# Performance work log

Hardware: AMD Instinct MI355X
Metric: run time of the kernel (lower is better)

Reference implementation:

```python
import jax, jax.numpy as jnp
import numpy as np

DIM = 768
HEADS = 12
HEAD_DIM = DIM // HEADS
HIDDEN = int(DIM * 2.0)
EPS = 1e-5


def layer_norm(x, g, b):
    mu = jnp.mean(x, axis=-1, keepdims=True)
    var = jnp.var(x, axis=-1, keepdims=True)
    return (x - mu) * jax.lax.rsqrt(var + EPS) * g + b


def setup_inputs() -> dict:
    key = jax.random.key(0)
    ks = jax.random.split(key, 10)
    B, N = 8, 1024
    s = 0.02
    return {
        "x": jax.random.normal(ks[0], (B, N, DIM), jnp.float32),
        "rpe_bias": jax.random.normal(ks[1], (HEADS, N, N), jnp.float32),
        # weights stored as (in, out); equals torch Linear weight transposed
        "qkv_w": jax.random.normal(ks[2], (DIM, 3 * DIM), jnp.float32) * s,
        "proj_w": jax.random.normal(ks[3], (DIM, DIM), jnp.float32) * s,
        "proj_b": jnp.zeros((DIM,), jnp.float32),
        "ln1_g": jnp.ones((DIM,), jnp.float32),
        "ln1_b": jnp.zeros((DIM,), jnp.float32),
        "ln2_g": jnp.ones((DIM,), jnp.float32),
        "ln2_b": jnp.zeros((DIM,), jnp.float32),
        "fc1_w": jax.random.normal(ks[4], (DIM, HIDDEN), jnp.float32) * s,
        "fc1_b": jnp.zeros((HIDDEN,), jnp.float32),
        "fc2_w": jax.random.normal(ks[5], (HIDDEN, DIM), jnp.float32) * s,
        "fc2_b": jnp.zeros((DIM,), jnp.float32),
    }


def reference(x, rpe_bias, qkv_w, proj_w, proj_b, ln1_g, ln1_b, ln2_g, ln2_b,
              fc1_w, fc1_b, fc2_w, fc2_b):
    B, N, C = x.shape
    scale = HEAD_DIM ** -0.5

    # ---- attention branch (pre-norm) ----
    h = layer_norm(x, ln1_g, ln1_b)
    qkv = h @ qkv_w                                   # [B,N,3C]
    qkv = qkv.reshape(B, N, 3, HEADS, HEAD_DIM)
    q = jnp.transpose(qkv[:, :, 0], (0, 2, 1, 3))     # [B,H,N,D]
    k = jnp.transpose(qkv[:, :, 1], (0, 2, 1, 3))
    v = jnp.transpose(qkv[:, :, 2], (0, 2, 1, 3))
    attn = jnp.einsum('bhnd,bhmd->bhnm', q, k) * scale + rpe_bias[None]
    attn = jax.nn.softmax(attn, axis=-1)
    o = jnp.einsum('bhnm,bhmd->bhnd', attn, v)        # [B,H,N,D]
    o = jnp.transpose(o, (0, 2, 1, 3)).reshape(B, N, C)
    x = x + (o @ proj_w + proj_b)

    # ---- MLP branch (pre-norm) ----
    h = layer_norm(x, ln2_g, ln2_b)
    h = jax.nn.gelu(h @ fc1_w + fc1_b, approximate=False)
    x = x + (h @ fc2_w + fc2_b)
    return x
```

## Files before the change

kernel.cpp:

```cpp
#include <hip/hip_runtime.h>

typedef __bf16 bf16;
typedef __bf16 bf16x8 __attribute__((ext_vector_type(8)));
typedef float f32x4 __attribute__((ext_vector_type(4)));

#define DIM 768
#define HEADS 12
#define HD 64
#define HIDDEN 1536
#define BB 8
#define NN 1024
#define ROWS (BB*NN)

__device__ __forceinline__ void gload_lds16(const void* g, void* l) {
  __builtin_amdgcn_global_load_lds(
      (const __attribute__((address_space(1))) void*)g,
      (__attribute__((address_space(3))) void*)l, 16, 0, 0);
}

__global__ __launch_bounds__(256) void ln_kernel(
    const float* __restrict__ x, const float* __restrict__ gw,
    const float* __restrict__ bw, bf16* __restrict__ out)
{
  const int row = blockIdx.x;
  const int tid = threadIdx.x;
  const float* xr = x + (size_t)row * DIM;
  float v0 = xr[tid], v1 = xr[tid + 256], v2 = xr[tid + 512];
  float s1 = v0 + v1 + v2;
  float s2 = v0*v0 + v1*v1 + v2*v2;
#pragma unroll
  for (int off = 1; off < 64; off <<= 1) {
    s1 += __shfl_xor(s1, off);
    s2 += __shfl_xor(s2, off);
  }
  __shared__ float red[8];
  const int w = tid >> 6, lane = tid & 63;
  if (lane == 0) { red[w] = s1; red[4 + w] = s2; }
  __syncthreads();
  s1 = red[0] + red[1] + red[2] + red[3];
  s2 = red[4] + red[5] + red[6] + red[7];
  const float mu = s1 * (1.f / DIM);
  const float rstd = rsqrtf(s2 * (1.f / DIM) - mu * mu + 1e-5f);
  bf16* orow = out + (size_t)row * DIM;
  orow[tid]       = (bf16)((v0 - mu) * rstd * gw[tid]       + bw[tid]);
  orow[tid + 256] = (bf16)((v1 - mu) * rstd * gw[tid + 256] + bw[tid + 256]);
  orow[tid + 512] = (bf16)((v2 - mu) * rstd * gw[tid + 512] + bw[tid + 512]);
}

__global__ void wtrans_kernel(const float* __restrict__ in, bf16* __restrict__ out,
                              int K, int N)
{
  __shared__ float t[32][33];
  const int tx = threadIdx.x, ty = threadIdx.y;
  const int n0 = blockIdx.x * 32, k0 = blockIdx.y * 32;
#pragma unroll
  for (int i = 0; i < 32; i += 8)
    t[ty + i][tx] = in[(size_t)(k0 + ty + i) * N + n0 + tx];
  __syncthreads();
#pragma unroll
  for (int i = 0; i < 32; i += 8)
    out[(size_t)(n0 + ty + i) * K + k0 + tx] = (bf16)t[tx][ty + i];
}

template<int EPI>
__global__ __launch_bounds__(256, 2) void gemm128(
    const bf16* __restrict__ A, const bf16* __restrict__ Bt,
    int M, int N, int K,
    const float* __restrict__ bias, const float* __restrict__ resid,
    void* __restrict__ o0, void* __restrict__ o1, void* __restrict__ o2)
{
  __shared__ bf16 sA[128 * 64];
  __shared__ bf16 sB[128 * 64];
  const int tid = threadIdx.x;
  const int lane = tid & 63, w = tid >> 6;
  const int wrow = w >> 1, wcol = w & 1;
  const int m0 = blockIdx.y * 128, n0 = blockIdx.x * 128;
  const int l15 = lane & 15, l4 = lane >> 4;

  f32x4 acc[4][4] = {};

  const int crow = lane >> 3;
  const int cbyte = (lane & 7) * 16;
  const int ksteps = K >> 6;
  for (int kt = 0; kt < ksteps; ++kt) {
    const int k0 = kt << 6;
    __syncthreads();
#pragma unroll
    for (int c2 = 0; c2 < 4; ++c2) {
      const int c = (w << 2) + c2;
      const int r = (c << 3) + crow;
      gload_lds16((const char*)(A + (size_t)(m0 + r) * K + k0) + cbyte,
                  (char*)sA + c * 1024);
      gload_lds16((const char*)(Bt + (size_t)(n0 + r) * K + k0) + cbyte,
                  (char*)sB + c * 1024);
    }
    __syncthreads();
#pragma unroll
    for (int kk = 0; kk < 64; kk += 32) {
      bf16x8 af[4], bfv[4];
#pragma unroll
      for (int mf = 0; mf < 4; ++mf)
        af[mf] = *(const bf16x8*)(sA + (wrow * 64 + mf * 16 + l15) * 64 + kk + l4 * 8);
#pragma unroll
      for (int nf = 0; nf < 4; ++nf)
        bfv[nf] = *(const bf16x8*)(sB + (wcol * 64 + nf * 16 + l15) * 64 + kk + l4 * 8);
#pragma unroll
      for (int mf = 0; mf < 4; ++mf)
#pragma unroll
        for (int nf = 0; nf < 4; ++nf)
          acc[mf][nf] = __builtin_amdgcn_mfma_f32_16x16x32_bf16(af[mf], bfv[nf], acc[mf][nf], 0, 0, 0);
    }
  }

#pragma unroll
  for (int mf = 0; mf < 4; ++mf) {
    const int rbase = m0 + wrow * 64 + mf * 16 + l4 * 4;
#pragma unroll
    for (int nf = 0; nf < 4; ++nf) {
      const int colbase = n0 + wcol * 64 + nf * 16;
      const int col = colbase + l15;
      if constexpr (EPI == 0) {
        const int seg = colbase / 768;
        const int hh_ = (colbase - seg * 768) >> 6;
        const int dd = (colbase & 63) + l15;
        const int b_ = rbase >> 10;
        const int ns = rbase & 1023;
        const size_t gh = (size_t)(b_ * HEADS + hh_);
        bf16* Qb = (bf16*)o0; bf16* Kb = (bf16*)o1; bf16* Vtb = (bf16*)o2;
        if (seg == 0) {
#pragma unroll
          for (int rg = 0; rg < 4; ++rg)
            Qb[(gh * NN + ns + rg) * HD + dd] = (bf16)(acc[mf][nf][rg] * 0.125f);
        } else if (seg == 1) {
#pragma unroll
          for (int rg = 0; rg < 4; ++rg)
            Kb[(gh * NN + ns + rg) * HD + dd] = (bf16)acc[mf][nf][rg];
        } else {
          union { ushort4 u4; unsigned short us[4]; } pk;
#pragma unroll
          for (int rg = 0; rg < 4; ++rg)
            pk.us[rg] = __builtin_bit_cast(unsigned short, (bf16)acc[mf][nf][rg]);
          *(ushort4*)(Vtb + (gh * HD + dd) * NN + ns) = pk.u4;
        }
      } else if constexpr (EPI == 1 || EPI == 3) {
        float* outp = (float*)o0;
#pragma unroll
        for (int rg = 0; rg < 4; ++rg) {
          const size_t idx = (size_t)(rbase + rg) * N + col;
          outp[idx] = acc[mf][nf][rg] + bias[col] + resid[idx];
        }
      } else {
        bf16* outp = (bf16*)o0;
#pragma unroll
        for (int rg = 0; rg < 4; ++rg) {
          float v = acc[mf][nf][rg] + bias[col];
          float gl = 0.5f * v * (1.0f + erff(v * 0.70710678118654752f));
          outp[(size_t)(rbase + rg) * N + col] = (bf16)gl;
        }
      }
    }
  }
}

__global__ __launch_bounds__(256, 2) void attn_kernel(
    const bf16* __restrict__ Qb, const bf16* __restrict__ Kb,
    const bf16* __restrict__ Vtb, const float* __restrict__ rpe,
    bf16* __restrict__ o_attn)
{
  __shared__ bf16 sK[64 * 64];
  __shared__ bf16 sV[64 * 64];
  __shared__ bf16 sP[4 * 16 * 64];
  const int tid = threadIdx.x;
  const int lane = tid & 63, w = tid >> 6;
  const int l15 = lane & 15, l4 = lane >> 4;
  const int bid = blockIdx.x;
  const int g = bid >> 4, qt = bid & 15;
  const int b_ = g / HEADS, h_ = g % HEADS;
  const int qbase = qt * 64 + w * 16;

  bf16x8 qf[2];
  {
    const bf16* qp = Qb + ((size_t)g * NN + qbase + l15) * HD + l4 * 8;
    qf[0] = *(const bf16x8*)qp;
    qf[1] = *(const bf16x8*)(qp + 32);
  }

  f32x4 oacc[4] = {};
  float m_r[4] = {-1e30f, -1e30f, -1e30f, -1e30f};
  float l_r[4] = {};
  const float* rpe_h = rpe + (size_t)h_ * NN * NN;

  const int crow = lane >> 3;
  const int scol = ((lane & 7) * 16) ^ ((crow & 7) << 4);

  for (int kv0 = 0; kv0 < NN; kv0 += 64) {
    __syncthreads();
#pragma unroll
    for (int c2 = 0; c2 < 2; ++c2) {
      const int c = w * 2 + c2;
      const int r = c * 8 + crow;
      gload_lds16((const char*)(Kb + ((size_t)g * NN + kv0) * HD) + r * 128 + scol,
                  (char*)sK + c * 1024);
      gload_lds16((const char*)(Vtb + ((size_t)g * HD + r) * NN + kv0) + scol,
                  (char*)sV + c * 1024);
    }
    __syncthreads();

    f32x4 s[4] = {};
#pragma unroll
    for (int kh = 0; kh < 2; ++kh) {
#pragma unroll
      for (int nf = 0; nf < 4; ++nf) {
        const int n_ = nf * 16 + l15;
        const bf16x8 kf = *(const bf16x8*)((const char*)sK + n_ * 128 +
                            (((kh * 32 + l4 * 8) * 2) ^ ((n_ & 7) << 4)));
        s[nf] = __builtin_amdgcn_mfma_f32_16x16x32_bf16(qf[kh], kf, s[nf], 0, 0, 0);
      }
    }
    float rm[4] = {-1e30f, -1e30f, -1e30f, -1e30f};
#pragma unroll
    for (int nf = 0; nf < 4; ++nf) {
      const int kvc = kv0 + nf * 16 + l15;
#pragma unroll
      for (int rg = 0; rg < 4; ++rg) {
        const int qr = qbase + l4 * 4 + rg;
        float v = s[nf][rg] + rpe_h[(size_t)qr * NN + kvc];
        s[nf][rg] = v;
        rm[rg] = fmaxf(rm[rg], v);
      }
    }
#pragma unroll
    for (int off = 1; off <= 8; off <<= 1)
#pragma unroll
      for (int rg = 0; rg < 4; ++rg)
        rm[rg] = fmaxf(rm[rg], __shfl_xor(rm[rg], off));
    float al[4];
#pragma unroll
    for (int rg = 0; rg < 4; ++rg) {
      const float mn = fmaxf(m_r[rg], rm[rg]);
      al[rg] = __expf(m_r[rg] - mn);
      m_r[rg] = mn;
    }
    float rs[4] = {};
#pragma unroll
    for (int nf = 0; nf < 4; ++nf)
#pragma unroll
      for (int rg = 0; rg < 4; ++rg) {
        const float p = __expf(s[nf][rg] - m_r[rg]);
        rs[rg] += p;
        const int r = l4 * 4 + rg;
        const int cb = (nf * 16 + l15) * 2;
        *(bf16*)((char*)sP + w * 2048 + r * 128 + (cb ^ ((r & 7) << 4))) = (bf16)p;
      }
#pragma unroll
    for (int off = 1; off <= 8; off <<= 1)
#pragma unroll
      for (int rg = 0; rg < 4; ++rg)
        rs[rg] += __shfl_xor(rs[rg], off);
#pragma unroll
    for (int rg = 0; rg < 4; ++rg)
      l_r[rg] = l_r[rg] * al[rg] + rs[rg];
#pragma unroll
    for (int df = 0; df < 4; ++df)
#pragma unroll
      for (int rg = 0; rg < 4; ++rg)
        oacc[df][rg] *= al[rg];
    __syncthreads();

#pragma unroll
    for (int kh = 0; kh < 2; ++kh) {
      const bf16x8 pf = *(const bf16x8*)((const char*)sP + w * 2048 + l15 * 128 +
                          (((kh * 32 + l4 * 8) * 2) ^ ((l15 & 7) << 4)));
#pragma unroll
      for (int df = 0; df < 4; ++df) {
        const int d_ = df * 16 + l15;
        const bf16x8 vf = *(const bf16x8*)((const char*)sV + d_ * 128 +
                            (((kh * 32 + l4 * 8) * 2) ^ ((d_ & 7) << 4)));
        oacc[df] = __builtin_amdgcn_mfma_f32_16x16x32_bf16(pf, vf, oacc[df], 0, 0, 0);
      }
    }
  }

#pragma unroll
  for (int rg = 0; rg < 4; ++rg) {
    const float inv = 1.0f / l_r[rg];
    const int qr = qbase + l4 * 4 + rg;
    bf16* orow = o_attn + ((size_t)(b_ * NN) + qr) * DIM + h_ * HD;
#pragma unroll
    for (int df = 0; df < 4; ++df)
      orow[df * 16 + l15] = (bf16)(oacc[df][rg] * inv);
  }
}

extern "C" void kernel_launch(void* const* d_in, const int* in_sizes, int n_in,
                              void* d_out, int out_size, void* d_ws, size_t ws_size,
                              hipStream_t stream)
{
  const float* x      = (const float*)d_in[0];
  const float* rpe    = (const float*)d_in[1];
  const float* qkv_w  = (const float*)d_in[2];
  const float* proj_w = (const float*)d_in[3];
  const float* proj_b = (const float*)d_in[4];
  const float* ln1_g  = (const float*)d_in[5];
  const float* ln1_b  = (const float*)d_in[6];
  const float* ln2_g  = (const float*)d_in[7];
  const float* ln2_b  = (const float*)d_in[8];
  const float* fc1_w  = (const float*)d_in[9];
  const float* fc1_b  = (const float*)d_in[10];
  const float* fc2_w  = (const float*)d_in[11];
  const float* fc2_b  = (const float*)d_in[12];
  float* out = (float*)d_out;

  char* ws = (char*)d_ws;
  size_t off = 0;
  bf16* qkv_wT  = (bf16*)(ws + off); off += (size_t)2304 * 768 * 2;
  bf16* proj_wT = (bf16*)(ws + off); off += (size_t)768 * 768 * 2;
  bf16* fc1_wT  = (bf16*)(ws + off); off += (size_t)1536 * 768 * 2;
  bf16* fc2_wT  = (bf16*)(ws + off); off += (size_t)768 * 1536 * 2;
  bf16* hbuf    = (bf16*)(ws + off); off += (size_t)ROWS * DIM * 2;
  bf16* Qb      = (bf16*)(ws + off); off += (size_t)96 * NN * HD * 2;
  bf16* Kb      = (bf16*)(ws + off); off += (size_t)96 * NN * HD * 2;
  bf16* Vtb     = (bf16*)(ws + off); off += (size_t)96 * HD * NN * 2;
  float* x1     = (float*)(ws + off); off += (size_t)ROWS * DIM * 4;
  bf16* o_attn = hbuf;
  bf16* h2 = Qb;
  bf16* hh = Kb;

  dim3 tb(32, 8);
  wtrans_kernel<<<dim3(2304 / 32, 768 / 32), tb, 0, stream>>>(qkv_w, qkv_wT, 768, 2304);
  wtrans_kernel<<<dim3(768 / 32, 768 / 32),  tb, 0, stream>>>(proj_w, proj_wT, 768, 768);
  wtrans_kernel<<<dim3(1536 / 32, 768 / 32), tb, 0, stream>>>(fc1_w, fc1_wT, 768, 1536);
  wtrans_kernel<<<dim3(768 / 32, 1536 / 32), tb, 0, stream>>>(fc2_w, fc2_wT, 1536, 768);

  ln_kernel<<<ROWS, 256, 0, stream>>>(x, ln1_g, ln1_b, hbuf);
  gemm128<0><<<dim3(2304 / 128, ROWS / 128), 256, 0, stream>>>(
      hbuf, qkv_wT, ROWS, 2304, 768, nullptr, nullptr, (void*)Qb, (void*)Kb, (void*)Vtb);
  attn_kernel<<<96 * 16, 256, 0, stream>>>(Qb, Kb, Vtb, rpe, o_attn);
  gemm128<1><<<dim3(768 / 128, ROWS / 128), 256, 0, stream>>>(
      o_attn, proj_wT, ROWS, 768, 768, proj_b, x, (void*)x1, nullptr, nullptr);
  ln_kernel<<<ROWS, 256, 0, stream>>>(x1, ln2_g, ln2_b, h2);
  gemm128<2><<<dim3(1536 / 128, ROWS / 128), 256, 0, stream>>>(
      h2, fc1_wT, ROWS, 1536, 768, fc1_b, nullptr, (void*)hh, nullptr, nullptr);
  gemm128<3><<<dim3(768 / 128, ROWS / 128), 256, 0, stream>>>(
      hh, fc2_wT, ROWS, 768, 1536, fc2_b, x1, (void*)out, nullptr, nullptr);
}
```

Baseline: 415.5 us.

## Convert rpe bias to bf16 and double-buffer K/V tiles in attention

A new kernel converts the fp32 relative-position bias to bf16 once per call into reused workspace. The attention kernel then reads the bf16 bias, which halves the bias traffic that is repeated for each of the 8 batches. The attention loop now double-buffers the K/V LDS tiles, prefetching the next tile while computing the current one, and drops one barrier per iteration. It also loads the bias values into registers ahead of the QK MFMAs and raises the launch-bounds occupancy hint from 2 to 4. The costs are an extra conversion pass over the bias, twice the K/V LDS footprint and a small loss of bias precision.

```diff
diff --git a/kernel.cpp b/kernel.cpp
--- a/kernel.cpp
+++ b/kernel.cpp
@@ -16,6 +16,22 @@
   __builtin_amdgcn_global_load_lds(
       (const __attribute__((address_space(1))) void*)g,
       (__attribute__((address_space(3))) void*)l, 16, 0, 0);
+}
+
+__global__ __launch_bounds__(256) void rpe_cvt_kernel(
+    const float* __restrict__ in, bf16* __restrict__ out)
+{
+  const size_t total = (size_t)HEADS * NN * NN;
+  const size_t stride = (size_t)gridDim.x * 256 * 4;
+  for (size_t i = ((size_t)blockIdx.x * 256 + threadIdx.x) * 4; i < total; i += stride) {
+    const float4 v = *(const float4*)(in + i);
+    ushort4 u;
+    u.x = __builtin_bit_cast(unsigned short, (bf16)v.x);
+    u.y = __builtin_bit_cast(unsigned short, (bf16)v.y);
+    u.z = __builtin_bit_cast(unsigned short, (bf16)v.z);
+    u.w = __builtin_bit_cast(unsigned short, (bf16)v.w);
+    *(ushort4*)(out + i) = u;
+  }
 }
 
 __global__ __launch_bounds__(256) void ln_kernel(
@@ -162,13 +178,13 @@
   }
 }
 
-__global__ __launch_bounds__(256, 2) void attn_kernel(
+__global__ __launch_bounds__(256, 4) void attn_kernel(
     const bf16* __restrict__ Qb, const bf16* __restrict__ Kb,
-    const bf16* __restrict__ Vtb, const float* __restrict__ rpe,
+    const bf16* __restrict__ Vtb, const bf16* __restrict__ rpeb,
     bf16* __restrict__ o_attn)
 {
-  __shared__ bf16 sK[64 * 64];
-  __shared__ bf16 sV[64 * 64];
+  __shared__ bf16 sK[2][64 * 64];
+  __shared__ bf16 sV[2][64 * 64];
   __shared__ bf16 sP[4 * 16 * 64];
   const int tid = threadIdx.x;
   const int lane = tid & 63, w = tid >> 6;
@@ -188,23 +204,36 @@
   f32x4 oacc[4] = {};
   float m_r[4] = {-1e30f, -1e30f, -1e30f, -1e30f};
   float l_r[4] = {};
-  const float* rpe_h = rpe + (size_t)h_ * NN * NN;
+  const bf16* rpe_h = rpeb + (size_t)h_ * NN * NN;
 
   const int crow = lane >> 3;
   const int scol = ((lane & 7) * 16) ^ ((crow & 7) << 4);
+  const int cc = w * 2;
+
+#define STAGE(buf, kv0s) do {                                                      \
+    _Pragma("unroll")                                                              \
+    for (int c2 = 0; c2 < 2; ++c2) {                                               \
+      const int c = cc + c2;                                                       \
+      const int r = c * 8 + crow;                                                  \
+      gload_lds16((const char*)(Kb + ((size_t)g * NN + (kv0s)) * HD) + r * 128 + scol, \
+                  (char*)sK[buf] + c * 1024);                                      \
+      gload_lds16((const char*)(Vtb + ((size_t)g * HD + r) * NN + (kv0s)) + scol,  \
+                  (char*)sV[buf] + c * 1024);                                      \
+    } } while (0)
+
+  STAGE(0, 0);
+  __syncthreads();
+  int cur = 0;
 
   for (int kv0 = 0; kv0 < NN; kv0 += 64) {
-    __syncthreads();
-#pragma unroll
-    for (int c2 = 0; c2 < 2; ++c2) {
-      const int c = w * 2 + c2;
-      const int r = c * 8 + crow;
-      gload_lds16((const char*)(Kb + ((size_t)g * NN + kv0) * HD) + r * 128 + scol,
-                  (char*)sK + c * 1024);
-      gload_lds16((const char*)(Vtb + ((size_t)g * HD + r) * NN + kv0) + scol,
-                  (char*)sV + c * 1024);
-    }
-    __syncthreads();
+    if (kv0 + 64 < NN) STAGE(cur ^ 1, kv0 + 64);
+
+    float rv[4][4];
+#pragma unroll
+    for (int nf = 0; nf < 4; ++nf)
+#pragma unroll
+      for (int rg = 0; rg < 4; ++rg)
+        rv[nf][rg] = (float)rpe_h[(size_t)(qbase + l4 * 4 + rg) * NN + kv0 + nf * 16 + l15];
 
     f32x4 s[4] = {};
 #pragma unroll
@@ -212,23 +241,20 @@
 #pragma unroll
       for (int nf = 0; nf < 4; ++nf) {
         const int n_ = nf * 16 + l15;
-        const bf16x8 kf = *(const bf16x8*)((const char*)sK + n_ * 128 +
+        const bf16x8 kf = *(const bf16x8*)((const char*)sK[cur] + n_ * 128 +
                             (((kh * 32 + l4 * 8) * 2) ^ ((n_ & 7) << 4)));
         s[nf] = __builtin_amdgcn_mfma_f32_16x16x32_bf16(qf[kh], kf, s[nf], 0, 0, 0);
       }
     }
     float rm[4] = {-1e30f, -1e30f, -1e30f, -1e30f};
 #pragma unroll
-    for (int nf = 0; nf < 4; ++nf) {
-      const int kvc = kv0 + nf * 16 + l15;
+    for (int nf = 0; nf < 4; ++nf)
 #pragma unroll
       for (int rg = 0; rg < 4; ++rg) {
-        const int qr = qbase + l4 * 4 + rg;
-        float v = s[nf][rg] + rpe_h[(size_t)qr * NN + kvc];
+        float v = s[nf][rg] + rv[nf][rg];
         s[nf][rg] = v;
         rm[rg] = fmaxf(rm[rg], v);
       }
-    }
 #pragma unroll
     for (int off = 1; off <= 8; off <<= 1)
 #pragma unroll
@@ -265,7 +291,6 @@
 #pragma unroll
       for (int rg = 0; rg < 4; ++rg)
         oacc[df][rg] *= al[rg];
-    __syncthreads();
 
 #pragma unroll
     for (int kh = 0; kh < 2; ++kh) {
@@ -274,12 +299,15 @@
 #pragma unroll
       for (int df = 0; df < 4; ++df) {
         const int d_ = df * 16 + l15;
-        const bf16x8 vf = *(const bf16x8*)((const char*)sV + d_ * 128 +
+        const bf16x8 vf = *(const bf16x8*)((const char*)sV[cur] + d_ * 128 +
                             (((kh * 32 + l4 * 8) * 2) ^ ((d_ & 7) << 4)));
         oacc[df] = __builtin_amdgcn_mfma_f32_16x16x32_bf16(pf, vf, oacc[df], 0, 0, 0);
       }
     }
-  }
+    __syncthreads();
+    cur ^= 1;
+  }
+#undef STAGE
 
 #pragma unroll
   for (int rg = 0; rg < 4; ++rg) {
@@ -325,17 +353,19 @@
   bf16* o_attn = hbuf;
   bf16* h2 = Qb;
   bf16* hh = Kb;
+  bf16* rpeb = (bf16*)x1;
 
   dim3 tb(32, 8);
   wtrans_kernel<<<dim3(2304 / 32, 768 / 32), tb, 0, stream>>>(qkv_w, qkv_wT, 768, 2304);
   wtrans_kernel<<<dim3(768 / 32, 768 / 32),  tb, 0, stream>>>(proj_w, proj_wT, 768, 768);
   wtrans_kernel<<<dim3(1536 / 32, 768 / 32), tb, 0, stream>>>(fc1_w, fc1_wT, 768, 1536);
   wtrans_kernel<<<dim3(768 / 32, 1536 / 32), tb, 0, stream>>>(fc2_w, fc2_wT, 1536, 768);
+  rpe_cvt_kernel<<<3072, 256, 0, stream>>>(rpe, rpeb);
 
   ln_kernel<<<ROWS, 256, 0, stream>>>(x, ln1_g, ln1_b, hbuf);
   gemm128<0><<<dim3(2304 / 128, ROWS / 128), 256, 0, stream>>>(
       hbuf, qkv_wT, ROWS, 2304, 768, nullptr, nullptr, (void*)Qb, (void*)Kb, (void*)Vtb);
-  attn_kernel<<<96 * 16, 256, 0, stream>>>(Qb, Kb, Vtb, rpe, o_attn);
+  attn_kernel<<<96 * 16, 256, 0, stream>>>(Qb, Kb, Vtb, rpeb, o_attn);
   gemm128<1><<<dim3(768 / 128, ROWS / 128), 256, 0, stream>>>(
       o_attn, proj_wT, ROWS, 768, 768, proj_b, x, (void*)x1, nullptr, nullptr);
   ln_kernel<<<ROWS, 256, 0, stream>>>(x1, ln2_g, ln2_b, h2);
```

Measured after the change: 399.3 us. -3.9%, faster.
